# Optimization experiments

Measured on AMD Instinct MI355X. Metric: run time of the kernel, lower is better.

The kernel has to match this reference:

```python
import jax, jax.numpy as jnp
import numpy as np

L, B, D = 1024, 24, 512


def setup_inputs() -> dict:
    key = jax.random.key(0)
    ks = jax.random.split(key, 9)
    s = 1.0 / np.sqrt(D)
    return {
        "v": jax.random.normal(ks[0], (L, B, D), dtype=jnp.float32),
        "h0": jax.random.normal(ks[1], (B, D), dtype=jnp.float32),
        "V": jax.random.normal(ks[2], (B, D), dtype=jnp.float32),
        "Wp": jax.random.normal(ks[3], (D, D), dtype=jnp.float32) * s,
        "Wp_": jax.random.normal(ks[4], (D, D), dtype=jnp.float32) * s,
        "w_ih": jax.random.normal(ks[5], (3 * D, D), dtype=jnp.float32) * s,
        "w_hh": jax.random.normal(ks[6], (3 * D, D), dtype=jnp.float32) * s,
        "b_ih": jax.random.normal(ks[7], (3 * D,), dtype=jnp.float32) * s,
        "b_hh": jax.random.normal(ks[8], (3 * D,), dtype=jnp.float32) * s,
    }


def reference(v, h0, V, Wp, Wp_, w_ih, w_hh, b_ih, b_hh):
    # v: [l, b, d]. Precompute both projections once (original wastefully
    # recomputes Wp_(v) per step; the math is identical).
    Wpv_all = jnp.einsum('lbd,hd->lbh', v, Wp)    # per-step query proj
    Wpvp = jnp.einsum('lbd,hd->lbh', v, Wp_)      # shared key proj

    def step(h, wpv_i):
        # additive attention over all l positions
        x = jnp.tanh(wpv_i[None, :, :] + Wpvp)           # [l, b, h]
        s = jnp.einsum('lbh,bh->bl', x, V)               # scores
        a = jax.nn.softmax(s, axis=1)                    # [b, l]
        c = jnp.einsum('bl,lbd->bd', a, v)               # context [b, d]
        # torch.nn.GRUCell math
        gi = c @ w_ih.T + b_ih
        gh = h @ w_hh.T + b_hh
        i_r, i_z, i_n = jnp.split(gi, 3, axis=1)
        h_r, h_z, h_n = jnp.split(gh, 3, axis=1)
        r = jax.nn.sigmoid(i_r + h_r)
        z = jax.nn.sigmoid(i_z + h_z)
        n = jnp.tanh(i_n + r * h_n)
        h_new = (1.0 - z) * n + z * h
        return h_new, h_new

    _, hs = jax.lax.scan(step, h0, Wpv_all)              # hs: [l, b, d]
    # dropout is identity in eval mode
    return hs
```

## Files before the change

### kernel.cpp

```cpp
#include <hip/hip_runtime.h>
#include <math.h>


__launch_bounds__(256, 2)
__global__ void gemm_abt_kernel(const float* __restrict__ A, const float* __restrict__ B,
                                float* __restrict__ out, int K, int N,
                                const float* __restrict__ bias, int do_tanh) {
  __shared__ __align__(16) float As[16][136];
  __shared__ __align__(16) float Bs[16][136];
  const int m0 = blockIdx.y * 128, n0 = blockIdx.x * 128;
  const int tid = threadIdx.x;
  const int tm = (tid & 15) * 8, tn = (tid >> 4) * 8;
  const int srow = tid & 127, scol = (tid >> 7) * 8;
  const float* Ap = A + (size_t)(m0 + srow) * K + scol;
  const float* Bp = B + (size_t)(n0 + srow) * K + scol;
  float acc[8][8] = {{0.f}};
  for (int k0 = 0; k0 < K; k0 += 16) {
    const float4 a0 = *(const float4*)(Ap + k0);
    const float4 a1 = *(const float4*)(Ap + k0 + 4);
    const float4 b0 = *(const float4*)(Bp + k0);
    const float4 b1 = *(const float4*)(Bp + k0 + 4);
    __syncthreads();
    As[scol + 0][srow] = a0.x; As[scol + 1][srow] = a0.y;
    As[scol + 2][srow] = a0.z; As[scol + 3][srow] = a0.w;
    As[scol + 4][srow] = a1.x; As[scol + 5][srow] = a1.y;
    As[scol + 6][srow] = a1.z; As[scol + 7][srow] = a1.w;
    Bs[scol + 0][srow] = b0.x; Bs[scol + 1][srow] = b0.y;
    Bs[scol + 2][srow] = b0.z; Bs[scol + 3][srow] = b0.w;
    Bs[scol + 4][srow] = b1.x; Bs[scol + 5][srow] = b1.y;
    Bs[scol + 6][srow] = b1.z; Bs[scol + 7][srow] = b1.w;
    __syncthreads();
#pragma unroll
    for (int kk = 0; kk < 16; ++kk) {
      const float4 av0 = *(const float4*)&As[kk][tm];
      const float4 av1 = *(const float4*)&As[kk][tm + 4];
      const float4 bv0 = *(const float4*)&Bs[kk][tn];
      const float4 bv1 = *(const float4*)&Bs[kk][tn + 4];
      const float ar[8] = {av0.x, av0.y, av0.z, av0.w, av1.x, av1.y, av1.z, av1.w};
      const float br[8] = {bv0.x, bv0.y, bv0.z, bv0.w, bv1.x, bv1.y, bv1.z, bv1.w};
#pragma unroll
      for (int r = 0; r < 8; ++r)
#pragma unroll
        for (int c = 0; c < 8; ++c)
          acc[r][c] = fmaf(ar[r], br[c], acc[r][c]);
    }
  }
#pragma unroll
  for (int r = 0; r < 8; ++r) {
    float* o = out + (size_t)(m0 + tm + r) * N + n0 + tn;
#pragma unroll
    for (int c = 0; c < 8; ++c) {
      float val = acc[r][c];
      if (bias) val += bias[n0 + tn + c];
      if (do_tanh) val = tanhf(val);
      o[c] = val;
    }
  }
}

__launch_bounds__(256, 3)
__global__ void attn_kernel(const float* __restrict__ tq, const float* __restrict__ tk,
                            const float* __restrict__ Vv, const float* __restrict__ v,
                            float* __restrict__ Cout) {
  const int b = blockIdx.y;
  const int it = blockIdx.x;
  const int tid = threadIdx.x;
  const int wave = tid >> 6, lane = tid & 63;
  const int h8 = lane * 8;
  __shared__ __align__(16) float sm[4][1024];
  __shared__ __align__(16) float red[4][4][512];
  __shared__ float inv_s[4];

  float q[4][8], vp[4][8];
  {
    const float* vvp = Vv + (size_t)b * 512 + h8;
    const float4 v0 = *(const float4*)vvp;
    const float4 v1 = *(const float4*)(vvp + 4);
    const float vv[8] = {v0.x, v0.y, v0.z, v0.w, v1.x, v1.y, v1.z, v1.w};
#pragma unroll
    for (int ii = 0; ii < 4; ++ii) {
      const float* qp = tq + ((size_t)(it * 4 + ii) * 24 + b) * 512 + h8;
      const float4 q0 = *(const float4*)qp;
      const float4 q1 = *(const float4*)(qp + 4);
      q[ii][0] = q0.x; q[ii][1] = q0.y; q[ii][2] = q0.z; q[ii][3] = q0.w;
      q[ii][4] = q1.x; q[ii][5] = q1.y; q[ii][6] = q1.z; q[ii][7] = q1.w;
#pragma unroll
      for (int j = 0; j < 8; ++j)
        vp[ii][j] = vv[j] * (1.0f - q[ii][j] * q[ii][j]);
    }
  }

  for (int l = wave; l < 1024; l += 4) {
    const float* kp = tk + ((size_t)l * 24 + b) * 512 + h8;
    const float4 k0 = *(const float4*)kp;
    const float4 k1 = *(const float4*)(kp + 4);
    const float kkv[8] = {k0.x, k0.y, k0.z, k0.w, k1.x, k1.y, k1.z, k1.w};
    float acc0 = 0.f, acc1 = 0.f, acc2 = 0.f, acc3 = 0.f;
#pragma unroll
    for (int j = 0; j < 8; ++j) {
      const float w = kkv[j];
      acc0 = fmaf(vp[0][j] * w, __builtin_amdgcn_rcpf(fmaf(q[0][j], w, 1.0f)), acc0);
      acc1 = fmaf(vp[1][j] * w, __builtin_amdgcn_rcpf(fmaf(q[1][j], w, 1.0f)), acc1);
      acc2 = fmaf(vp[2][j] * w, __builtin_amdgcn_rcpf(fmaf(q[2][j], w, 1.0f)), acc2);
      acc3 = fmaf(vp[3][j] * w, __builtin_amdgcn_rcpf(fmaf(q[3][j], w, 1.0f)), acc3);
    }
#pragma unroll
    for (int mask = 32; mask; mask >>= 1) {
      acc0 += __shfl_xor(acc0, mask, 64);
      acc1 += __shfl_xor(acc1, mask, 64);
      acc2 += __shfl_xor(acc2, mask, 64);
      acc3 += __shfl_xor(acc3, mask, 64);
    }
    if (lane == 0) {
      sm[0][l] = acc0; sm[1][l] = acc1; sm[2][l] = acc2; sm[3][l] = acc3;
    }
  }
  __syncthreads();

  {
    float* row = sm[wave];
    float m = -1e30f;
    for (int t = lane; t < 1024; t += 64) m = fmaxf(m, row[t]);
#pragma unroll
    for (int mask = 32; mask; mask >>= 1) m = fmaxf(m, __shfl_xor(m, mask, 64));
    float s = 0.f;
    for (int t = lane; t < 1024; t += 64) {
      const float e = __expf(row[t] - m);
      row[t] = e;
      s += e;
    }
#pragma unroll
    for (int mask = 32; mask; mask >>= 1) s += __shfl_xor(s, mask, 64);
    if (lane == 0) inv_s[wave] = 1.0f / s;
  }
  __syncthreads();

  float ca[4][8] = {{0.f}};
  const int l0 = wave * 256;
  for (int l = l0; l < l0 + 256; ++l) {
    const float* vrow = v + ((size_t)l * 24 + b) * 512 + h8;
    const float4 x0 = *(const float4*)vrow;
    const float4 x1 = *(const float4*)(vrow + 4);
    const float a0 = sm[0][l], a1 = sm[1][l], a2 = sm[2][l], a3 = sm[3][l];
    const float xv[8] = {x0.x, x0.y, x0.z, x0.w, x1.x, x1.y, x1.z, x1.w};
#pragma unroll
    for (int j = 0; j < 8; ++j) {
      ca[0][j] = fmaf(a0, xv[j], ca[0][j]);
      ca[1][j] = fmaf(a1, xv[j], ca[1][j]);
      ca[2][j] = fmaf(a2, xv[j], ca[2][j]);
      ca[3][j] = fmaf(a3, xv[j], ca[3][j]);
    }
  }
#pragma unroll
  for (int ii = 0; ii < 4; ++ii) {
    *(float4*)&red[wave][ii][h8]     = make_float4(ca[ii][0], ca[ii][1], ca[ii][2], ca[ii][3]);
    *(float4*)&red[wave][ii][h8 + 4] = make_float4(ca[ii][4], ca[ii][5], ca[ii][6], ca[ii][7]);
  }
  __syncthreads();
  {
    const int ii = tid >> 6;
    const int d0 = (tid & 63) * 8;
    float4 s0 = *(const float4*)&red[0][ii][d0];
    float4 s1 = *(const float4*)&red[0][ii][d0 + 4];
#pragma unroll
    for (int w = 1; w < 4; ++w) {
      const float4 r0 = *(const float4*)&red[w][ii][d0];
      const float4 r1 = *(const float4*)&red[w][ii][d0 + 4];
      s0.x += r0.x; s0.y += r0.y; s0.z += r0.z; s0.w += r0.w;
      s1.x += r1.x; s1.y += r1.y; s1.z += r1.z; s1.w += r1.w;
    }
    const float inv = inv_s[ii];
    s0.x *= inv; s0.y *= inv; s0.z *= inv; s0.w *= inv;
    s1.x *= inv; s1.y *= inv; s1.z *= inv; s1.w *= inv;
    float* o = Cout + ((size_t)(it * 4 + ii) * 24 + b) * 512 + d0;
    *(float4*)o = s0;
    *(float4*)(o + 4) = s1;
  }
}

union HPack {
  unsigned long long u;
  struct { float f; unsigned tag; } s;
};

__launch_bounds__(512, 1)
__global__ void gru_persist_kernel(const float* __restrict__ Gi_c,
                                   const float* __restrict__ w_hh,
                                   const float* __restrict__ b_hh,
                                   const float* __restrict__ h0,
                                   unsigned long long* __restrict__ hb0,
                                   unsigned long long* __restrict__ hb1,
                                   float* __restrict__ out, int gstep0) {
  const int g  = blockIdx.x & 7;
  const int sl = blockIdx.x >> 3;
  const int t = threadIdx.x;
  const int w = t >> 6;
  const int l = t & 63;
  const int og = l >> 3;
  const int kc = l & 7;
  const int d_w = w * 8 + og;
  const int dglob = sl * 64 + d_w;
  const bool pub = (kc == 0);

  __shared__ __align__(16) float h_lds[2][544];

  float wreg[3][64];
#pragma unroll
  for (int gg = 0; gg < 3; ++gg) {
    const float* wr = w_hh + (size_t)(gg * 512 + dglob) * 512 + kc * 64;
#pragma unroll
    for (int j = 0; j < 64; j += 4) {
      const float4 wv = *(const float4*)(wr + j);
      wreg[gg][j] = wv.x; wreg[gg][j + 1] = wv.y; wreg[gg][j + 2] = wv.z; wreg[gg][j + 3] = wv.w;
    }
  }
  const float bias_r = b_hh[dglob];
  const float bias_z = b_hh[512 + dglob];
  const float bias_n = b_hh[1024 + dglob];

  if (gstep0 == 0 && t < 192) {
    const int q = t >> 6, d = t & 63;
    const int bg = g * 3 + q;
    HPack p;
    p.s.f = h0[(size_t)bg * 512 + sl * 64 + d];
    p.s.tag = 1u;
    __hip_atomic_store(hb1 + (size_t)bg * 512 + sl * 64 + d, p.u,
                       __ATOMIC_RELAXED, __HIP_MEMORY_SCOPE_AGENT);
  }

  float hq[3];
  HPack pf;
  pf.u = __hip_atomic_load(((gstep0 & 1) ? hb0 : hb1) + (size_t)(g * 3) * 512 + t,
                           __ATOMIC_RELAXED, __HIP_MEMORY_SCOPE_AGENT);

  for (int il = 0; il < 128; ++il) {
    const int gs = gstep0 + il;
#pragma unroll
    for (int q = 0; q < 3; ++q) {
      const int bg = g * 3 + q;
      const unsigned want = (unsigned)(gs + 1);
      const unsigned long long* src = ((gs & 1) ? hb0 : hb1) + (size_t)bg * 512 + t;

      HPack p = pf;
      {
        const int gs_n = (q == 2) ? gs + 1 : gs;
        const int bg_n = (q == 2) ? g * 3 : bg + 1;
        pf.u = __hip_atomic_load(((gs_n & 1) ? hb0 : hb1) + (size_t)bg_n * 512 + t,
                                 __ATOMIC_RELAXED, __HIP_MEMORY_SCOPE_AGENT);
      }
      float gir = 0.f, giz = 0.f, gin = 0.f;
      if (pub) {
        const float* gi = Gi_c + ((size_t)il * 24 + bg) * 1536 + dglob;
        gir = gi[0]; giz = gi[512]; gin = gi[1024];
      }
      while (p.s.tag < want) {
        __builtin_amdgcn_s_sleep(1);
        p.u = __hip_atomic_load(src, __ATOMIC_RELAXED, __HIP_MEMORY_SCOPE_AGENT);
      }
      const int buf = (il + q) & 1;
      h_lds[buf][t + ((t >> 6) << 2)] = p.s.f;
      __syncthreads();
      if (il == 0 && pub) hq[q] = h_lds[buf][dglob + ((dglob >> 6) << 2)];

      const float* hbp = &h_lds[buf][kc * 68];
      float a0 = 0.f, a1 = 0.f, a2 = 0.f, b0 = 0.f, b1 = 0.f, b2 = 0.f;
#pragma unroll
      for (int j = 0; j < 64; j += 8) {
        const float4 h1 = *(const float4*)(hbp + j);
        const float4 h2 = *(const float4*)(hbp + j + 4);
        a0 = fmaf(h1.x, wreg[0][j], fmaf(h1.y, wreg[0][j+1], fmaf(h1.z, wreg[0][j+2], fmaf(h1.w, wreg[0][j+3], a0))));
        b0 = fmaf(h2.x, wreg[0][j+4], fmaf(h2.y, wreg[0][j+5], fmaf(h2.z, wreg[0][j+6], fmaf(h2.w, wreg[0][j+7], b0))));
        a1 = fmaf(h1.x, wreg[1][j], fmaf(h1.y, wreg[1][j+1], fmaf(h1.z, wreg[1][j+2], fmaf(h1.w, wreg[1][j+3], a1))));
        b1 = fmaf(h2.x, wreg[1][j+4], fmaf(h2.y, wreg[1][j+5], fmaf(h2.z, wreg[1][j+6], fmaf(h2.w, wreg[1][j+7], b1))));
        a2 = fmaf(h1.x, wreg[2][j], fmaf(h1.y, wreg[2][j+1], fmaf(h1.z, wreg[2][j+2], fmaf(h1.w, wreg[2][j+3], a2))));
        b2 = fmaf(h2.x, wreg[2][j+4], fmaf(h2.y, wreg[2][j+5], fmaf(h2.z, wreg[2][j+6], fmaf(h2.w, wreg[2][j+7], b2))));
      }
      float sr = a0 + b0, sz = a1 + b1, sn = a2 + b2;
#pragma unroll
      for (int mask = 1; mask <= 4; mask <<= 1) {
        sr += __shfl_xor(sr, mask, 64);
        sz += __shfl_xor(sz, mask, 64);
        sn += __shfl_xor(sn, mask, 64);
      }

      if (pub) {
        const float r = __builtin_amdgcn_rcpf(1.0f + __expf(-(gir + sr + bias_r)));
        const float z = __builtin_amdgcn_rcpf(1.0f + __expf(-(giz + sz + bias_z)));
        const float nx = gin + r * (sn + bias_n);
        const float e2 = __expf(-2.0f * fabsf(nx));
        const float tn = __builtin_copysignf((1.0f - e2) * __builtin_amdgcn_rcpf(1.0f + e2), nx);
        const float hn = (1.0f - z) * tn + z * hq[q];
        hq[q] = hn;
        HPack pw; pw.s.f = hn; pw.s.tag = (unsigned)(gs + 2);
        __hip_atomic_store(((gs & 1) ? hb1 : hb0) + (size_t)bg * 512 + dglob, pw.u,
                           __ATOMIC_RELAXED, __HIP_MEMORY_SCOPE_AGENT);
        out[((size_t)gs * 24 + bg) * 512 + dglob] = hn;
      }
    }
  }
}

extern "C" void kernel_launch(void* const* d_in, const int* in_sizes, int n_in,
                              void* d_out, int out_size, void* d_ws, size_t ws_size,
                              hipStream_t stream) {
  (void)in_sizes; (void)n_in; (void)out_size;
  const float* v    = (const float*)d_in[0];
  const float* h0   = (const float*)d_in[1];
  const float* Vv   = (const float*)d_in[2];
  const float* Wp   = (const float*)d_in[3];
  const float* Wp_  = (const float*)d_in[4];
  const float* w_ih = (const float*)d_in[5];
  const float* w_hh = (const float*)d_in[6];
  const float* b_ih = (const float*)d_in[7];
  const float* b_hh = (const float*)d_in[8];
  float* out = (float*)d_out;

  const bool full_tq = ws_size >= (size_t)126025728;
  float* ws   = (float*)d_ws;
  float* tk   = ws;
  float* tqF  = tk + (size_t)12582912;
  float* tq_c = tk + (size_t)12582912;
  float* C_c  = full_tq ? (tqF + (size_t)12582912) : (tq_c + (size_t)1572864);
  float* Gi_c = C_c + (size_t)1572864;
  unsigned long long* hb0 = (unsigned long long*)(Gi_c + (size_t)4718592);
  unsigned long long* hb1 = hb0 + (size_t)12288;

  hipMemsetAsync(hb0, 0, (size_t)2 * 12288 * sizeof(unsigned long long), stream);

  gemm_abt_kernel<<<dim3(4, 192), 256, 0, stream>>>(v, Wp_, tk, 512, 512, nullptr, 1);
  if (full_tq)
    gemm_abt_kernel<<<dim3(4, 192), 256, 0, stream>>>(v, Wp, tqF, 512, 512, nullptr, 1);

  for (int c = 0; c < 8; ++c) {
    const float* v_chunk = v + (size_t)c * 128 * 24 * 512;
    const float* tq_use;
    if (full_tq) {
      tq_use = tqF + (size_t)c * 128 * 24 * 512;
    } else {
      gemm_abt_kernel<<<dim3(4, 24), 256, 0, stream>>>(v_chunk, Wp, tq_c, 512, 512, nullptr, 1);
      tq_use = tq_c;
    }
    attn_kernel<<<dim3(32, 24), 256, 0, stream>>>(tq_use, tk, Vv, v, C_c);
    gemm_abt_kernel<<<dim3(12, 24), 256, 0, stream>>>(C_c, w_ih, Gi_c, 512, 1536, b_ih, 0);
    gru_persist_kernel<<<64, 512, 0, stream>>>(Gi_c, w_hh, b_hh, h0, hb0, hb1,
                                               out, c * 128);
  }
}
```

Before: 8.414 ms.

## Spread persistent GRU recurrence across more blocks with shorter per-thread dot products

The persistent GRU kernel now runs 128 blocks of 1024 threads instead of 64 blocks of 512. Each block owns 32 hidden outputs, and each output is reduced over 32 lanes with 16 weights per thread instead of 8 lanes with 64 weights. The goal is a shorter serial FMA chain per step and fewer weight registers per thread, which cuts per-step latency on the critical recurrence path. In exchange there are twice as many blocks polling the shared h buffers, a larger block-wide barrier, and a deeper shuffle reduction; the persistent spin-wait design also needs all 128 blocks to be co-resident.

```diff
diff --git a/kernel.cpp b/kernel.cpp
--- a/kernel.cpp
+++ b/kernel.cpp
@@ -183,7 +183,7 @@
   struct { float f; unsigned tag; } s;
 };
 
-__launch_bounds__(512, 1)
+__launch_bounds__(1024, 1)
 __global__ void gru_persist_kernel(const float* __restrict__ Gi_c,
                                    const float* __restrict__ w_hh,
                                    const float* __restrict__ b_hh,
@@ -193,45 +193,44 @@
                                    float* __restrict__ out, int gstep0) {
   const int g  = blockIdx.x & 7;
   const int sl = blockIdx.x >> 3;
-  const int t = threadIdx.x;
-  const int w = t >> 6;
-  const int l = t & 63;
-  const int og = l >> 3;
-  const int kc = l & 7;
-  const int d_w = w * 8 + og;
-  const int dglob = sl * 64 + d_w;
+  const int t  = threadIdx.x;
+  const int r  = t >> 5;
+  const int kc = t & 31;
+  const int dgr = sl * 32 + r;
   const bool pub = (kc == 0);
 
-  __shared__ __align__(16) float h_lds[2][544];
-
-  float wreg[3][64];
+  __shared__ __align__(16) float h_lds[2][640];
+
+  float wreg[3][16];
 #pragma unroll
   for (int gg = 0; gg < 3; ++gg) {
-    const float* wr = w_hh + (size_t)(gg * 512 + dglob) * 512 + kc * 64;
-#pragma unroll
-    for (int j = 0; j < 64; j += 4) {
+    const float* wr = w_hh + (size_t)(gg * 512 + dgr) * 512 + kc * 16;
+#pragma unroll
+    for (int j = 0; j < 16; j += 4) {
       const float4 wv = *(const float4*)(wr + j);
-      wreg[gg][j] = wv.x; wreg[gg][j + 1] = wv.y; wreg[gg][j + 2] = wv.z; wreg[gg][j + 3] = wv.w;
-    }
-  }
-  const float bias_r = b_hh[dglob];
-  const float bias_z = b_hh[512 + dglob];
-  const float bias_n = b_hh[1024 + dglob];
-
-  if (gstep0 == 0 && t < 192) {
-    const int q = t >> 6, d = t & 63;
+      wreg[gg][j] = wv.x; wreg[gg][j + 1] = wv.y;
+      wreg[gg][j + 2] = wv.z; wreg[gg][j + 3] = wv.w;
+    }
+  }
+  const float bias_r = b_hh[dgr];
+  const float bias_z = b_hh[512 + dgr];
+  const float bias_n = b_hh[1024 + dgr];
+
+  if (gstep0 == 0 && t < 96) {
+    const int q = t >> 5, d = t & 31;
     const int bg = g * 3 + q;
     HPack p;
-    p.s.f = h0[(size_t)bg * 512 + sl * 64 + d];
+    p.s.f = h0[(size_t)bg * 512 + sl * 32 + d];
     p.s.tag = 1u;
-    __hip_atomic_store(hb1 + (size_t)bg * 512 + sl * 64 + d, p.u,
+    __hip_atomic_store(hb1 + (size_t)bg * 512 + sl * 32 + d, p.u,
                        __ATOMIC_RELAXED, __HIP_MEMORY_SCOPE_AGENT);
   }
 
   float hq[3];
   HPack pf;
-  pf.u = __hip_atomic_load(((gstep0 & 1) ? hb0 : hb1) + (size_t)(g * 3) * 512 + t,
-                           __ATOMIC_RELAXED, __HIP_MEMORY_SCOPE_AGENT);
+  if (t < 512)
+    pf.u = __hip_atomic_load(((gstep0 & 1) ? hb0 : hb1) + (size_t)(g * 3) * 512 + t,
+                             __ATOMIC_RELAXED, __HIP_MEMORY_SCOPE_AGENT);
 
   for (int il = 0; il < 128; ++il) {
     const int gs = gstep0 + il;
@@ -239,62 +238,65 @@
     for (int q = 0; q < 3; ++q) {
       const int bg = g * 3 + q;
       const unsigned want = (unsigned)(gs + 1);
-      const unsigned long long* src = ((gs & 1) ? hb0 : hb1) + (size_t)bg * 512 + t;
-
-      HPack p = pf;
-      {
-        const int gs_n = (q == 2) ? gs + 1 : gs;
-        const int bg_n = (q == 2) ? g * 3 : bg + 1;
-        pf.u = __hip_atomic_load(((gs_n & 1) ? hb0 : hb1) + (size_t)bg_n * 512 + t,
-                                 __ATOMIC_RELAXED, __HIP_MEMORY_SCOPE_AGENT);
+      const int buf = (il + q) & 1;
+
+      if (t < 512) {
+        const unsigned long long* src = ((gs & 1) ? hb0 : hb1) + (size_t)bg * 512 + t;
+        HPack p = pf;
+        {
+          const int gs_n = (q == 2) ? gs + 1 : gs;
+          const int bg_n = (q == 2) ? g * 3 : bg + 1;
+          pf.u = __hip_atomic_load(((gs_n & 1) ? hb0 : hb1) + (size_t)bg_n * 512 + t,
+                                   __ATOMIC_RELAXED, __HIP_MEMORY_SCOPE_AGENT);
+        }
+        while (p.s.tag < want) {
+          p.u = __hip_atomic_load(src, __ATOMIC_RELAXED, __HIP_MEMORY_SCOPE_AGENT);
+          if (p.s.tag >= want) break;
+          __builtin_amdgcn_s_sleep(1);
+        }
+        h_lds[buf][t + ((t >> 4) << 2)] = p.s.f;
       }
       float gir = 0.f, giz = 0.f, gin = 0.f;
       if (pub) {
-        const float* gi = Gi_c + ((size_t)il * 24 + bg) * 1536 + dglob;
+        const float* gi = Gi_c + ((size_t)il * 24 + bg) * 1536 + dgr;
         gir = gi[0]; giz = gi[512]; gin = gi[1024];
       }
-      while (p.s.tag < want) {
-        __builtin_amdgcn_s_sleep(1);
-        p.u = __hip_atomic_load(src, __ATOMIC_RELAXED, __HIP_MEMORY_SCOPE_AGENT);
-      }
-      const int buf = (il + q) & 1;
-      h_lds[buf][t + ((t >> 6) << 2)] = p.s.f;
       __syncthreads();
-      if (il == 0 && pub) hq[q] = h_lds[buf][dglob + ((dglob >> 6) << 2)];
-
-      const float* hbp = &h_lds[buf][kc * 68];
-      float a0 = 0.f, a1 = 0.f, a2 = 0.f, b0 = 0.f, b1 = 0.f, b2 = 0.f;
-#pragma unroll
-      for (int j = 0; j < 64; j += 8) {
-        const float4 h1 = *(const float4*)(hbp + j);
-        const float4 h2 = *(const float4*)(hbp + j + 4);
-        a0 = fmaf(h1.x, wreg[0][j], fmaf(h1.y, wreg[0][j+1], fmaf(h1.z, wreg[0][j+2], fmaf(h1.w, wreg[0][j+3], a0))));
-        b0 = fmaf(h2.x, wreg[0][j+4], fmaf(h2.y, wreg[0][j+5], fmaf(h2.z, wreg[0][j+6], fmaf(h2.w, wreg[0][j+7], b0))));
-        a1 = fmaf(h1.x, wreg[1][j], fmaf(h1.y, wreg[1][j+1], fmaf(h1.z, wreg[1][j+2], fmaf(h1.w, wreg[1][j+3], a1))));
-        b1 = fmaf(h2.x, wreg[1][j+4], fmaf(h2.y, wreg[1][j+5], fmaf(h2.z, wreg[1][j+6], fmaf(h2.w, wreg[1][j+7], b1))));
-        a2 = fmaf(h1.x, wreg[2][j], fmaf(h1.y, wreg[2][j+1], fmaf(h1.z, wreg[2][j+2], fmaf(h1.w, wreg[2][j+3], a2))));
-        b2 = fmaf(h2.x, wreg[2][j+4], fmaf(h2.y, wreg[2][j+5], fmaf(h2.z, wreg[2][j+6], fmaf(h2.w, wreg[2][j+7], b2))));
-      }
-      float sr = a0 + b0, sz = a1 + b1, sn = a2 + b2;
-#pragma unroll
-      for (int mask = 1; mask <= 4; mask <<= 1) {
+      if (il == 0 && pub) hq[q] = h_lds[buf][dgr + ((dgr >> 4) << 2)];
+
+      const float* hbp = &h_lds[buf][kc * 20];
+      float hv[16];
+#pragma unroll
+      for (int j = 0; j < 16; j += 4) {
+        const float4 x = *(const float4*)(hbp + j);
+        hv[j] = x.x; hv[j + 1] = x.y; hv[j + 2] = x.z; hv[j + 3] = x.w;
+      }
+      float sr = 0.f, sz = 0.f, sn = 0.f;
+#pragma unroll
+      for (int j = 0; j < 16; ++j) {
+        sr = fmaf(hv[j], wreg[0][j], sr);
+        sz = fmaf(hv[j], wreg[1][j], sz);
+        sn = fmaf(hv[j], wreg[2][j], sn);
+      }
+#pragma unroll
+      for (int mask = 1; mask <= 16; mask <<= 1) {
         sr += __shfl_xor(sr, mask, 64);
         sz += __shfl_xor(sz, mask, 64);
         sn += __shfl_xor(sn, mask, 64);
       }
 
       if (pub) {
-        const float r = __builtin_amdgcn_rcpf(1.0f + __expf(-(gir + sr + bias_r)));
-        const float z = __builtin_amdgcn_rcpf(1.0f + __expf(-(giz + sz + bias_z)));
-        const float nx = gin + r * (sn + bias_n);
+        const float rg = __builtin_amdgcn_rcpf(1.0f + __expf(-(gir + sr + bias_r)));
+        const float zg = __builtin_amdgcn_rcpf(1.0f + __expf(-(giz + sz + bias_z)));
+        const float nx = gin + rg * (sn + bias_n);
         const float e2 = __expf(-2.0f * fabsf(nx));
         const float tn = __builtin_copysignf((1.0f - e2) * __builtin_amdgcn_rcpf(1.0f + e2), nx);
-        const float hn = (1.0f - z) * tn + z * hq[q];
+        const float hn = (1.0f - zg) * tn + zg * hq[q];
         hq[q] = hn;
         HPack pw; pw.s.f = hn; pw.s.tag = (unsigned)(gs + 2);
-        __hip_atomic_store(((gs & 1) ? hb1 : hb0) + (size_t)bg * 512 + dglob, pw.u,
+        __hip_atomic_store(((gs & 1) ? hb1 : hb0) + (size_t)bg * 512 + dgr, pw.u,
                            __ATOMIC_RELAXED, __HIP_MEMORY_SCOPE_AGENT);
-        out[((size_t)gs * 24 + bg) * 512 + dglob] = hn;
+        out[((size_t)gs * 24 + bg) * 512 + dgr] = hn;
       }
     }
   }
@@ -342,7 +344,7 @@
     }
     attn_kernel<<<dim3(32, 24), 256, 0, stream>>>(tq_use, tk, Vv, v, C_c);
     gemm_abt_kernel<<<dim3(12, 24), 256, 0, stream>>>(C_c, w_ih, Gi_c, 512, 1536, b_ih, 0);
-    gru_persist_kernel<<<64, 512, 0, stream>>>(Gi_c, w_hh, b_hh, h0, hb0, hb1,
-                                               out, c * 128);
+    gru_persist_kernel<<<128, 1024, 0, stream>>>(Gi_c, w_hh, b_hh, h0, hb0, hb1,
+                                                 out, c * 128);
   }
 }
```

Measured after the change: 8.852 ms. 5.2% more time.
